# Performance work log

Hardware: AMD Instinct MI355X
Metric: run time of the kernel (lower is better)

The kernel has to match this reference:

```python
import jax, jax.numpy as jnp
import numpy as np

NUM_USER = 100000
NUM_ITEM = 50000
N = NUM_USER + NUM_ITEM
DIM_FEAT = 512
DIM_LATENT = 64
NNZ = 2400000
N_LAYERS = 3


def setup_inputs() -> dict:
    key = jax.random.key(0)
    ks = jax.random.split(key, 6)
    features = jax.random.normal(ks[0], (NUM_ITEM, DIM_FEAT), dtype=jnp.float32)
    user_id_preference = jax.random.normal(ks[1], (NUM_USER, DIM_LATENT), dtype=jnp.float32)
    W = jax.random.normal(ks[2], (DIM_FEAT, DIM_LATENT), dtype=jnp.float32) * (1.0 / np.sqrt(DIM_FEAT))
    b = jnp.zeros((DIM_LATENT,), dtype=jnp.float32)
    rows = jax.random.randint(ks[3], (NNZ,), 0, N, dtype=jnp.int32)
    cols = jax.random.randint(ks[4], (NNZ,), 0, N, dtype=jnp.int32)
    vals = jax.random.uniform(ks[5], (NNZ,), dtype=jnp.float32)
    return {"features": features, "user_id_preference": user_id_preference,
            "W": W, "b": b, "rows": rows, "cols": cols, "vals": vals}


def reference(features, user_id_preference, W, b, rows, cols, vals):
    # MLP projection of item features: [num_item, dim_latent]
    temp_features = features @ W + b
    # Concat user preferences and projected item features: [N, dim_latent]
    all_emb = jnp.concatenate([user_id_preference, temp_features], axis=0)
    # F.normalize: row-wise L2 normalization with eps=1e-12
    nrm = jnp.sqrt(jnp.sum(all_emb * all_emb, axis=1, keepdims=True))
    all_emb = all_emb / jnp.maximum(nrm, 1e-12)
    # 3-layer sparse propagation: out[r] += v * emb[c]; accumulate layer mean
    embs_sum = all_emb
    for _ in range(N_LAYERS):
        gathered = all_emb[cols] * vals[:, None]  # [nnz, dim_latent]
        all_emb = jax.ops.segment_sum(gathered, rows, num_segments=N)
        embs_sum = embs_sum + all_emb
    light_out = embs_sum / (N_LAYERS + 1)
    users = light_out[:NUM_USER]
    items = light_out[NUM_USER:]
    return (users, items)
```

## Files before the change

kernel.cpp:

```cpp
#include <hip/hip_runtime.h>

#define NUSER 100000
#define NITEM 50000
#define NTOT  150000
#define DF    512
#define DL    64
#define NNZ_  2400000
#define NB    1172
#define NCHUNK 256
#define CHUNK  9375

typedef short bf16x8 __attribute__((ext_vector_type(8)));
typedef float f32x4  __attribute__((ext_vector_type(4)));

__device__ __forceinline__ unsigned short bf16r(float f) {
    unsigned u = __float_as_uint(f);
    return (unsigned short)((u + 0x7FFFu + ((u >> 16) & 1u)) >> 16);
}
__device__ __forceinline__ unsigned pack2(float lo, float hi) {
    return (unsigned)bf16r(lo) | ((unsigned)bf16r(hi) << 16);
}
__device__ __forceinline__ float blo(unsigned u) { return __uint_as_float(u << 16); }
__device__ __forceinline__ float bhi(unsigned u) { return __uint_as_float(u & 0xFFFF0000u); }

__global__ __launch_bounds__(256) void k_init(const float* __restrict__ up,
                                              const float* __restrict__ W,
                                              unsigned short* __restrict__ e0,
                                              unsigned short* __restrict__ Wtb) {
    int b = blockIdx.x;
    if (b < 128) {
        int idx = b * 256 + threadIdx.x;
        int k = idx >> 6, d = idx & 63;
        Wtb[d * DF + k] = bf16r(W[idx]);
        return;
    }
    int t = (b - 128) * 256 + threadIdx.x;
    float v = up[t];
    float ss = v * v;
    #pragma unroll
    for (int m = 32; m >= 1; m >>= 1) ss += __shfl_xor(ss, m, 64);
    float scale = 1.0f / fmaxf(sqrtf(ss), 1e-12f);
    e0[t] = bf16r(v * scale);
}

__global__ __launch_bounds__(256) void k_item(const float* __restrict__ F,
                                              const unsigned short* __restrict__ Wtb,
                                              const float* __restrict__ B,
                                              unsigned short* __restrict__ e0) {
    int t = threadIdx.x;
    int w = t >> 6, lane = t & 63;
    int g = lane >> 4;
    int c = lane & 15;
    int row_base = blockIdx.x * 64 + w * 16;

    int ar = row_base + c;
    if (ar >= NITEM) ar = NITEM - 1;
    const float* Frow = F + (size_t)ar * DF;

    f32x4 acc[4] = {};
    #pragma unroll 2
    for (int kc = 0; kc < DF; kc += 32) {
        int k0 = kc + g * 8;
        float4 f0 = *(const float4*)&Frow[k0];
        float4 f1 = *(const float4*)&Frow[k0 + 4];
        union { uint4 u; bf16x8 v; } a;
        a.u.x = pack2(f0.x, f0.y);
        a.u.y = pack2(f0.z, f0.w);
        a.u.z = pack2(f1.x, f1.y);
        a.u.w = pack2(f1.z, f1.w);
        #pragma unroll
        for (int ct = 0; ct < 4; ++ct) {
            union { uint4 u; bf16x8 v; } bb;
            bb.u = *(const uint4*)&Wtb[(size_t)(ct * 16 + c) * DF + k0];
            acc[ct] = __builtin_amdgcn_mfma_f32_16x16x32_bf16(a.v, bb.v, acc[ct], 0, 0, 0);
        }
    }

    #pragma unroll
    for (int ct = 0; ct < 4; ++ct) {
        float bc = B[ct * 16 + c];
        #pragma unroll
        for (int r = 0; r < 4; ++r) acc[ct][r] += bc;
    }
    float ssv[4];
    #pragma unroll
    for (int r = 0; r < 4; ++r) {
        float s = acc[0][r] * acc[0][r] + acc[1][r] * acc[1][r]
                + acc[2][r] * acc[2][r] + acc[3][r] * acc[3][r];
        #pragma unroll
        for (int m = 1; m <= 8; m <<= 1) s += __shfl_xor(s, m, 64);
        ssv[r] = 1.0f / fmaxf(sqrtf(s), 1e-12f);
    }
    #pragma unroll
    for (int r = 0; r < 4; ++r) {
        int gr = row_base + g * 4 + r;
        if (gr < NITEM) {
            size_t o = (size_t)(NUSER + gr) * DL + c;
            #pragma unroll
            for (int ct = 0; ct < 4; ++ct)
                e0[o + ct * 16] = bf16r(acc[ct][r] * ssv[r]);
        }
    }
}

__global__ __launch_bounds__(1024) void k_hist(const int* __restrict__ rows,
                                               int* __restrict__ cnt) {
    __shared__ int h[NB];
    int c = blockIdx.x, t = threadIdx.x;
    for (int i = t; i < NB; i += 1024) h[i] = 0;
    __syncthreads();
    int end = (c + 1) * CHUNK;
    for (int e = c * CHUNK + t; e < end; e += 1024)
        atomicAdd(&h[rows[e] >> 7], 1);
    __syncthreads();
    for (int i = t; i < NB; i += 1024) cnt[c * NB + i] = h[i];
}

__global__ __launch_bounds__(256) void k_scan1(const int* __restrict__ cnt,
                                               int* __restrict__ cntOff,
                                               int* __restrict__ binTot) {
    __shared__ int s[256];
    int b = blockIdx.x, t = threadIdx.x;
    int x = cnt[t * NB + b];
    s[t] = x;
    __syncthreads();
    #pragma unroll
    for (int off = 1; off < 256; off <<= 1) {
        int v = (t >= off) ? s[t - off] : 0;
        __syncthreads();
        s[t] += v;
        __syncthreads();
    }
    cntOff[t * NB + b] = s[t] - x;
    if (t == 255) binTot[b] = s[255];
}

__global__ __launch_bounds__(256) void k_scan2(const int* __restrict__ binTot,
                                               int* __restrict__ binBase) {
    __shared__ int s[256];
    __shared__ int carry;
    int t = threadIdx.x;
    if (t == 0) carry = 0;
    __syncthreads();
    for (int base = 0; base < NB; base += 256) {
        int idx = base + t;
        int x = (idx < NB) ? binTot[idx] : 0;
        s[t] = x;
        __syncthreads();
        #pragma unroll
        for (int off = 1; off < 256; off <<= 1) {
            int v = (t >= off) ? s[t - off] : 0;
            __syncthreads();
            s[t] += v;
            __syncthreads();
        }
        if (idx < NB) binBase[idx] = carry + s[t] - x;
        __syncthreads();
        if (t == 255) carry += s[255];
        __syncthreads();
    }
    if (t == 0) binBase[NB] = carry;
}

__global__ __launch_bounds__(1024) void k_scatter(const int* __restrict__ rows,
                                                  const int* __restrict__ cols,
                                                  const float* __restrict__ vals,
                                                  const int* __restrict__ cntOff,
                                                  const int* __restrict__ binBase,
                                                  int2* __restrict__ eb) {
    __shared__ int cur[NB];
    int c = blockIdx.x, t = threadIdx.x;
    for (int i = t; i < NB; i += 1024) cur[i] = binBase[i] + cntOff[c * NB + i];
    __syncthreads();
    int end = (c + 1) * CHUNK;
    for (int e = c * CHUNK + t; e < end; e += 1024) {
        int r = rows[e];
        int b = r >> 7;
        int pos = atomicAdd(&cur[b], 1);
        eb[pos] = make_int2(cols[e] | ((r & 127) << 18), __float_as_int(vals[e]));
    }
}

__global__ __launch_bounds__(256) void k_binsort(const int2* __restrict__ eb,
                                                 const int* __restrict__ binBase,
                                                 int2* __restrict__ eb2,
                                                 int2* __restrict__ rowSC) {
    __shared__ int h[128];
    __shared__ int s[128];
    int b = blockIdx.x, t = threadIdx.x;
    if (t < 128) h[t] = 0;
    __syncthreads();
    int base = binBase[b];
    int cnt  = binBase[b + 1] - base;
    for (int j = t; j < cnt; j += 256)
        atomicAdd(&h[eb[base + j].x >> 18], 1);
    __syncthreads();
    if (t < 128) s[t] = h[t];
    __syncthreads();
    #pragma unroll
    for (int off = 1; off < 128; off <<= 1) {
        int v = 0;
        if (t < 128 && t >= off) v = s[t - off];
        __syncthreads();
        if (t < 128) s[t] += v;
        __syncthreads();
    }
    if (t < 128) {
        int e = s[t] - h[t];
        int r = (b << 7) + t;
        if (r < NTOT) rowSC[r] = make_int2(base + e, h[t]);
        s[t] = e;
    }
    __syncthreads();
    for (int j = t; j < cnt; j += 256) {
        int2 e = eb[base + j];
        int rl = e.x >> 18;
        int pos = base + atomicAdd(&s[rl], 1);
        eb2[pos] = make_int2(e.x & 0x3FFFF, e.y);
    }
}

__global__ __launch_bounds__(256) void k_spmm_row(const int2* __restrict__ rowSC,
                                                  const int2* __restrict__ eb2,
                                                  const unsigned short* __restrict__ embIn,
                                                  unsigned short* __restrict__ embOut) {
    int gt = blockIdx.x * 256 + threadIdx.x;
    int r  = gt >> 4;
    if (r >= NTOT) return;
    int lq = threadIdx.x & 15;
    int2 sc = rowSC[r];
    int j = sc.x, end = sc.x + sc.y;
    float a0 = 0.f, a1 = 0.f, a2 = 0.f, a3 = 0.f;
    int doff = lq * 4;
    for (; j + 3 < end; j += 4) {
        int2 eA = eb2[j],     eB = eb2[j + 1];
        int2 eC = eb2[j + 2], eD = eb2[j + 3];
        uint2 mA = *(const uint2*)&embIn[eA.x * DL + doff];
        uint2 mB = *(const uint2*)&embIn[eB.x * DL + doff];
        uint2 mC = *(const uint2*)&embIn[eC.x * DL + doff];
        uint2 mD = *(const uint2*)&embIn[eD.x * DL + doff];
        float vA = __int_as_float(eA.y), vB = __int_as_float(eB.y);
        float vC = __int_as_float(eC.y), vD = __int_as_float(eD.y);
        a0 += vA * blo(mA.x); a1 += vA * bhi(mA.x); a2 += vA * blo(mA.y); a3 += vA * bhi(mA.y);
        a0 += vB * blo(mB.x); a1 += vB * bhi(mB.x); a2 += vB * blo(mB.y); a3 += vB * bhi(mB.y);
        a0 += vC * blo(mC.x); a1 += vC * bhi(mC.x); a2 += vC * blo(mC.y); a3 += vC * bhi(mC.y);
        a0 += vD * blo(mD.x); a1 += vD * bhi(mD.x); a2 += vD * blo(mD.y); a3 += vD * bhi(mD.y);
    }
    for (; j < end; ++j) {
        int2 e = eb2[j];
        uint2 m = *(const uint2*)&embIn[e.x * DL + doff];
        float v = __int_as_float(e.y);
        a0 += v * blo(m.x); a1 += v * bhi(m.x); a2 += v * blo(m.y); a3 += v * bhi(m.y);
    }
    uint2 o;
    o.x = pack2(a0, a1);
    o.y = pack2(a2, a3);
    *(uint2*)&embOut[r * DL + doff] = o;
}

__global__ __launch_bounds__(256) void k_spmm_last(const int2* __restrict__ rowSC,
                                                   const int2* __restrict__ eb2,
                                                   const unsigned short* __restrict__ e0,
                                                   const unsigned short* __restrict__ e1,
                                                   const unsigned short* __restrict__ e2,
                                                   float* __restrict__ out) {
    int gt = blockIdx.x * 256 + threadIdx.x;
    int r  = gt >> 4;
    if (r >= NTOT) return;
    int lq = threadIdx.x & 15;
    int2 sc = rowSC[r];
    int j = sc.x, end = sc.x + sc.y;
    float a0 = 0.f, a1 = 0.f, a2 = 0.f, a3 = 0.f;
    int doff = lq * 4;
    for (; j + 3 < end; j += 4) {
        int2 eA = eb2[j],     eB = eb2[j + 1];
        int2 eC = eb2[j + 2], eD = eb2[j + 3];
        uint2 mA = *(const uint2*)&e2[eA.x * DL + doff];
        uint2 mB = *(const uint2*)&e2[eB.x * DL + doff];
        uint2 mC = *(const uint2*)&e2[eC.x * DL + doff];
        uint2 mD = *(const uint2*)&e2[eD.x * DL + doff];
        float vA = __int_as_float(eA.y), vB = __int_as_float(eB.y);
        float vC = __int_as_float(eC.y), vD = __int_as_float(eD.y);
        a0 += vA * blo(mA.x); a1 += vA * bhi(mA.x); a2 += vA * blo(mA.y); a3 += vA * bhi(mA.y);
        a0 += vB * blo(mB.x); a1 += vB * bhi(mB.x); a2 += vB * blo(mB.y); a3 += vB * bhi(mB.y);
        a0 += vC * blo(mC.x); a1 += vC * bhi(mC.x); a2 += vC * blo(mC.y); a3 += vC * bhi(mC.y);
        a0 += vD * blo(mD.x); a1 += vD * bhi(mD.x); a2 += vD * blo(mD.y); a3 += vD * bhi(mD.y);
    }
    for (; j < end; ++j) {
        int2 e = eb2[j];
        uint2 m = *(const uint2*)&e2[e.x * DL + doff];
        float v = __int_as_float(e.y);
        a0 += v * blo(m.x); a1 += v * bhi(m.x); a2 += v * blo(m.y); a3 += v * bhi(m.y);
    }
    int o = r * DL + doff;
    uint2 ua = *(const uint2*)&e0[o];
    uint2 ub = *(const uint2*)&e1[o];
    uint2 uc = *(const uint2*)&e2[o];
    float4 res;
    res.x = 0.25f * (blo(ua.x) + blo(ub.x) + blo(uc.x) + a0);
    res.y = 0.25f * (bhi(ua.x) + bhi(ub.x) + bhi(uc.x) + a1);
    res.z = 0.25f * (blo(ua.y) + blo(ub.y) + blo(uc.y) + a2);
    res.w = 0.25f * (bhi(ua.y) + bhi(ub.y) + bhi(uc.y) + a3);
    *(float4*)&out[o] = res;
}

extern "C" void kernel_launch(void* const* d_in, const int* in_sizes, int n_in,
                              void* d_out, int out_size, void* d_ws, size_t ws_size,
                              hipStream_t stream) {
    const float* F    = (const float*)d_in[0];
    const float* UP   = (const float*)d_in[1];
    const float* W    = (const float*)d_in[2];
    const float* B    = (const float*)d_in[3];
    const int*   rows = (const int*)d_in[4];
    const int*   cols = (const int*)d_in[5];
    const float* vals = (const float*)d_in[6];
    float* out = (float*)d_out;

    unsigned short* e0 = (unsigned short*)d_ws;
    unsigned short* e1 = e0 + (size_t)NTOT * DL;
    unsigned short* e2 = e1 + (size_t)NTOT * DL;
    int2* eb      = (int2*)(e2 + (size_t)NTOT * DL);
    int2* eb2     = eb + (size_t)NNZ_;
    int2* rowSC   = eb2 + (size_t)NNZ_;
    int*  cnt     = (int*)(rowSC + NTOT);
    int*  cntOff  = cnt + (size_t)NCHUNK * NB;
    int*  binTot  = cntOff + (size_t)NCHUNK * NB;
    int*  binBase = binTot + NB;
    unsigned short* Wtb = (unsigned short*)(binBase + NB + 1);

    k_init<<<128 + (NUSER * DL) / 256, 256, 0, stream>>>(UP, W, e0, Wtb);
    k_item<<<(NITEM + 63) / 64, 256, 0, stream>>>(F, Wtb, B, e0);
    k_hist<<<NCHUNK, 1024, 0, stream>>>(rows, cnt);
    k_scan1<<<NB, 256, 0, stream>>>(cnt, cntOff, binTot);
    k_scan2<<<1, 256, 0, stream>>>(binTot, binBase);
    k_scatter<<<NCHUNK, 1024, 0, stream>>>(rows, cols, vals, cntOff, binBase, eb);
    k_binsort<<<NB, 256, 0, stream>>>(eb, binBase, eb2, rowSC);

    int spmm_blocks = (NTOT * 16 + 255) / 256;
    k_spmm_row<<<spmm_blocks, 256, 0, stream>>>(rowSC, eb2, e0, e1);
    k_spmm_row<<<spmm_blocks, 256, 0, stream>>>(rowSC, eb2, e1, e2);
    k_spmm_last<<<spmm_blocks, 256, 0, stream>>>(rowSC, eb2, e0, e1, e2, out);
}
```

Measured before the change: 311.6 us.

## Split item GEMM K dimension across waves with shared-memory reduction

The item projection kernel now gives each block 16 rows, and its four waves each handle a quarter of the 512-long K dimension. Partial MFMA accumulators are combined through shared memory before the bias, normalization and store. This launches four times as many blocks and shortens each wave's serial K loop, aiming for more memory-level parallelism on the feature read. In exchange it adds a shared-memory round trip, a barrier, and three idle waves during the epilogue. The row bounds checks are dropped because 50000 divides evenly by 16.

```diff
diff --git a/kernel.cpp b/kernel.cpp
--- a/kernel.cpp
+++ b/kernel.cpp
@@ -47,20 +47,20 @@
                                               const unsigned short* __restrict__ Wtb,
                                               const float* __restrict__ B,
                                               unsigned short* __restrict__ e0) {
+    __shared__ float red[3][64][20];
     int t = threadIdx.x;
     int w = t >> 6, lane = t & 63;
     int g = lane >> 4;
     int c = lane & 15;
-    int row_base = blockIdx.x * 64 + w * 16;
-
-    int ar = row_base + c;
-    if (ar >= NITEM) ar = NITEM - 1;
-    const float* Frow = F + (size_t)ar * DF;
+    int row_base = blockIdx.x * 16;
+
+    const float* Frow = F + (size_t)(row_base + c) * DF;
+    int kbase = w * 128;
 
     f32x4 acc[4] = {};
-    #pragma unroll 2
-    for (int kc = 0; kc < DF; kc += 32) {
-        int k0 = kc + g * 8;
+    #pragma unroll
+    for (int kc = 0; kc < 128; kc += 32) {
+        int k0 = kbase + kc + g * 8;
         float4 f0 = *(const float4*)&Frow[k0];
         float4 f1 = *(const float4*)&Frow[k0 + 4];
         union { uint4 u; bf16x8 v; } a;
@@ -76,6 +76,23 @@
         }
     }
 
+    if (w > 0) {
+        #pragma unroll
+        for (int ct = 0; ct < 4; ++ct)
+            *(f32x4*)&red[w - 1][lane][ct * 4] = acc[ct];
+    }
+    __syncthreads();
+    if (w != 0) return;
+
+    #pragma unroll
+    for (int i = 0; i < 3; ++i) {
+        #pragma unroll
+        for (int ct = 0; ct < 4; ++ct) {
+            f32x4 p = *(const f32x4*)&red[i][lane][ct * 4];
+            acc[ct] += p;
+        }
+    }
+
     #pragma unroll
     for (int ct = 0; ct < 4; ++ct) {
         float bc = B[ct * 16 + c];
@@ -94,12 +111,10 @@
     #pragma unroll
     for (int r = 0; r < 4; ++r) {
         int gr = row_base + g * 4 + r;
-        if (gr < NITEM) {
-            size_t o = (size_t)(NUSER + gr) * DL + c;
-            #pragma unroll
-            for (int ct = 0; ct < 4; ++ct)
-                e0[o + ct * 16] = bf16r(acc[ct][r] * ssv[r]);
-        }
+        size_t o = (size_t)(NUSER + gr) * DL + c;
+        #pragma unroll
+        for (int ct = 0; ct < 4; ++ct)
+            e0[o + ct * 16] = bf16r(acc[ct][r] * ssv[r]);
     }
 }
 
@@ -329,7 +344,7 @@
     unsigned short* Wtb = (unsigned short*)(binBase + NB + 1);
 
     k_init<<<128 + (NUSER * DL) / 256, 256, 0, stream>>>(UP, W, e0, Wtb);
-    k_item<<<(NITEM + 63) / 64, 256, 0, stream>>>(F, Wtb, B, e0);
+    k_item<<<NITEM / 16, 256, 0, stream>>>(F, Wtb, B, e0);
     k_hist<<<NCHUNK, 1024, 0, stream>>>(rows, cnt);
     k_scan1<<<NB, 256, 0, stream>>>(cnt, cntOff, binTot);
     k_scan2<<<1, 256, 0, stream>>>(binTot, binBase);
```

Result: no change. 308.8 us (-0.9%).
